# Kernel tuning notes

Hardware: AMD Instinct MI355X
Metric: run time of the kernel (lower is better)

## Reference

```python
import jax, jax.numpy as jnp
from jax import lax
import numpy as np

B, DIM, NH, H, W = 4, 256, 8, 32, 32
HEAD_DIM = DIM // NH          # 32
KEY_DIM = HEAD_DIM // 2       # attn_ratio = 0.5 -> 16
QKV_OUT = DIM + 2 * NH * KEY_DIM  # 512
SCALE = KEY_DIM ** -0.5


def setup_inputs() -> dict:
    key = jax.random.key(0)
    ks = jax.random.split(key, 11)
    w = lambda k, shape, s=0.05: jax.random.normal(k, shape, jnp.float32) * s
    return {
        "x": jax.random.normal(ks[0], (B, DIM, H, W), jnp.float32),
        "qkv_w": w(ks[1], (QKV_OUT, DIM)),
        "qkv_b": w(ks[2], (QKV_OUT,)),
        "proj_w": w(ks[3], (DIM, DIM)),
        "proj_b": w(ks[4], (DIM,)),
        "pe_w": w(ks[5], (DIM, 1, 3, 3)),
        "pe_b": w(ks[6], (DIM,)),
        "g1_w": w(ks[7], (DIM // 2, DIM)),
        "g1_b": w(ks[8], (DIM // 2,)),
        "g2_w": w(ks[9], (1, DIM // 2)),
        "g2_b": w(ks[10], (1,)),
    }


def conv1x1(x, w, b):
    # fused Conv2d(1x1, bias=False)+BN -> pointwise matmul + bias
    return jnp.einsum('bchw,oc->bohw', x, w) + b[None, :, None, None]


def reference(x, qkv_w, qkv_b, proj_w, proj_b, pe_w, pe_b, g1_w, g1_b, g2_w, g2_b):
    Bx, C, Hh, Ww = x.shape
    N = Hh * Ww
    qkv = conv1x1(x, qkv_w, qkv_b).reshape(Bx, NH, 2 * KEY_DIM + HEAD_DIM, N)
    q = qkv[:, :, :KEY_DIM]                   # [B, nh, key_dim, N]
    k = qkv[:, :, KEY_DIM:2 * KEY_DIM]        # [B, nh, key_dim, N]
    v = qkv[:, :, 2 * KEY_DIM:]               # [B, nh, head_dim, N]

    # attn = q^T @ k * scale  -> [B, nh, N, N]
    attn = jnp.einsum('bhdn,bhdm->bhnm', q, k) * SCALE

    # learned gate -> scalar dynamic k = floor(N * mean(sigmoid(...)))
    g = jax.nn.sigmoid(conv1x1(jax.nn.relu(conv1x1(x, g1_w, g1_b)), g2_w, g2_b))
    dyn_k = jnp.floor(N * jnp.mean(g)).astype(jnp.int32)

    # rank-based top-k mask (jit-friendly equivalent of topk+scatter):
    # keep entries whose descending rank along the last dim is < dyn_k
    order = jnp.argsort(-attn, axis=-1)       # positions sorted by score desc
    ranks = jnp.argsort(order, axis=-1)       # rank of each position
    attn = jnp.where(ranks < dyn_k, attn, -jnp.inf)
    attn = jax.nn.softmax(attn, axis=-1)

    out = jnp.einsum('bhdn,bhmn->bhdm', v, attn).reshape(Bx, C, Hh, Ww)

    # depthwise 3x3 positional-encoding conv on v reshaped to the image grid
    v_img = v.reshape(Bx, C, Hh, Ww)
    pe = lax.conv_general_dilated(
        v_img, pe_w, window_strides=(1, 1), padding=((1, 1), (1, 1)),
        dimension_numbers=('NCHW', 'OIHW', 'NCHW'), feature_group_count=C,
    ) + pe_b[None, :, None, None]

    return conv1x1(out + pe, proj_w, proj_b)
```

## Files before the change

### kernel.cpp

```cpp
#include <hip/hip_runtime.h>
#include <math.h>

#define NTOK 1024
#define CAP 64

#define LDS_FENCE() asm volatile("s_waitcnt lgkmcnt(0)" ::: "memory")

typedef __bf16 bf16x8 __attribute__((ext_vector_type(8)));
typedef unsigned short u16x8 __attribute__((ext_vector_type(8)));
typedef unsigned short u16x4 __attribute__((ext_vector_type(4)));
typedef float f32x4 __attribute__((ext_vector_type(4)));

__device__ __forceinline__ unsigned short f2bf(float f) {
  unsigned int u = __float_as_uint(f);
  return (unsigned short)((u + 0x7fffu + ((u >> 16) & 1u)) >> 16);
}


template<int OC, int OCB, int P, bool RELU, bool VCAST>
__global__ __launch_bounds__(256) void conv1x1_kernel(const float* __restrict__ in,
    const float* __restrict__ w, const float* __restrict__ bias, float* __restrict__ out,
    unsigned short* __restrict__ vbf) {
  constexpr int PB = NTOK / (256 * P);
  int bid = blockIdx.x;
  const int pb = bid % PB; bid /= PB;
  const int ocb = bid % (OC / OCB); const int b = bid / (OC / OCB);
  const int tid = threadIdx.x;
  const int p0 = pb * 256 * P + tid * P;
  const float* inb = in + (size_t)b * 256 * NTOK + p0;
  const float* wrow = w + (size_t)ocb * OCB * 256;

  float acc[OCB][P];
  #pragma unroll
  for (int j = 0; j < OCB; j++)
    #pragma unroll
    for (int i = 0; i < P; i++) acc[j][i] = 0.f;

  #pragma unroll 2
  for (int c0 = 0; c0 < 256; c0 += 4) {
    float4 wl[OCB];
    #pragma unroll
    for (int j = 0; j < OCB; j++) wl[j] = *(const float4*)&wrow[j * 256 + c0];
    #pragma unroll
    for (int cc = 0; cc < 4; cc++) {
      float xr[P];
      if constexpr (P == 4) {
        float4 t = *(const float4*)&inb[(size_t)(c0 + cc) * NTOK];
        xr[0] = t.x; xr[1] = t.y; xr[2] = t.z; xr[3] = t.w;
      } else if constexpr (P == 2) {
        float2 t = *(const float2*)&inb[(size_t)(c0 + cc) * NTOK];
        xr[0] = t.x; xr[1] = t.y;
      } else {
        xr[0] = inb[(size_t)(c0 + cc) * NTOK];
      }
      #pragma unroll
      for (int j = 0; j < OCB; j++) {
        const float wjc = ((const float*)&wl[j])[cc];
        #pragma unroll
        for (int i = 0; i < P; i++) acc[j][i] = fmaf(wjc, xr[i], acc[j][i]);
      }
    }
  }
  #pragma unroll
  for (int j = 0; j < OCB; j++) {
    const int oc = ocb * OCB + j;
    const float bv = bias[oc];
    float r[P];
    #pragma unroll
    for (int i = 0; i < P; i++) {
      float v = acc[j][i] + bv;
      if (RELU) v = fmaxf(v, 0.f);
      r[i] = v;
    }
    float* op = out + ((size_t)b * OC + oc) * NTOK + p0;
    if constexpr (P == 4) *(float4*)op = make_float4(r[0], r[1], r[2], r[3]);
    else if constexpr (P == 2) *(float2*)op = make_float2(r[0], r[1]);
    else *op = r[0];
    if constexpr (VCAST) {
      if ((oc & 63) >= 32) {
        const int c = (oc >> 6) * 32 + (oc & 63) - 32;
        unsigned short* vp = vbf + ((size_t)b * 256 + c) * NTOK + p0;
        #pragma unroll
        for (int i = 0; i < P; i++) vp[i] = f2bf(r[i]);
      }
    }
  }
}

__global__ __launch_bounds__(256) void gate2_kernel(const float* __restrict__ gx,
    const float* __restrict__ g2_w, const float* __restrict__ g2_b, double* __restrict__ part) {
  const int idx = blockIdx.x * 256 + threadIdx.x;
  const int b = idx >> 10, p = idx & 1023;
  float acc = g2_b[0];
  const float* gb = gx + (size_t)b * 128 * NTOK + p;
  #pragma unroll 4
  for (int j = 0; j < 128; j++) acc = fmaf(g2_w[j], gb[(size_t)j * NTOK], acc);
  float g = 1.f / (1.f + expf(-acc));
  __shared__ double red[256];
  red[threadIdx.x] = (double)g;
  __syncthreads();
  for (int s = 128; s > 0; s >>= 1) {
    if (threadIdx.x < s) red[threadIdx.x] += red[threadIdx.x + s];
    __syncthreads();
  }
  if (threadIdx.x == 0) part[blockIdx.x] = red[0];
}

__global__ __launch_bounds__(512) void attn_kernel(const float* __restrict__ qkv,
    const unsigned short* __restrict__ vbf,
    const double* __restrict__ part, float* __restrict__ out_attn) {
  const int tid = threadIdx.x;
  const int lane = tid & 63, wv = tid >> 6;
  int bid = blockIdx.x;
  const int mb = bid & 127; bid >>= 7;
  const int h = bid & 7; const int b = bid >> 3;

  double dsum = 0.0;
  #pragma unroll
  for (int i = 0; i < 16; i++) dsum += part[i];
  int dk = (int)floor(1024.0 * (dsum / 4096.0));
  const int dyn_k = dk < 1 ? 1 : (dk > NTOK ? NTOK : dk);

  const float* base = qkv + (size_t)(b * 512 + h * 64) * NTOK;

  __shared__ union RowU { float f[1028]; unsigned short pa[1032]; } rows[8];
  __shared__ float invs[8];
  __shared__ union UU {
    struct {
      int hist[8][64];
      int cnt[8];
      float Bv[8]; int Bn[8];
      struct { float v; int n; } cand[8][CAP];
    } sel;
    float pvred[2][4][8][17];
  } u;

  {
    const float2* k2 = (const float2*)(base + 16 * NTOK);
    const float* qb = base + mb * 8;
    float a0[8], a1[8];
    #pragma unroll
    for (int r = 0; r < 8; r++) { a0[r] = 0.f; a1[r] = 0.f; }
    #pragma unroll
    for (int d = 0; d < 16; d++) {
      float2 kk = k2[d * 512 + tid];
      #pragma unroll
      for (int r = 0; r < 8; r++) {
        const float qv = qb[(size_t)d * NTOK + r];
        a0[r] = fmaf(qv, kk.x, a0[r]);
        a1[r] = fmaf(qv, kk.y, a1[r]);
      }
    }
    #pragma unroll
    for (int r = 0; r < 8; r++)
      ((float2*)rows[r].f)[tid] = make_float2(a0[r] * 0.25f, a1[r] * 0.25f);
  }
  __syncthreads();

  {
    const int r = wv;
    float* smrow = rows[r].f;
    float v[16];
    {
      float4 f0 = ((const float4*)smrow)[lane];
      float4 f1 = ((const float4*)smrow)[64 + lane];
      float4 f2 = ((const float4*)smrow)[128 + lane];
      float4 f3 = ((const float4*)smrow)[192 + lane];
      v[0]=f0.x; v[1]=f0.y; v[2]=f0.z; v[3]=f0.w;
      v[4]=f1.x; v[5]=f1.y; v[6]=f1.z; v[7]=f1.w;
      v[8]=f2.x; v[9]=f2.y; v[10]=f2.z; v[11]=f2.w;
      v[12]=f3.x; v[13]=f3.y; v[14]=f3.z; v[15]=f3.w;
    }
    float mn = v[0], mx = v[0];
    #pragma unroll
    for (int i = 1; i < 16; i++) { mn = fminf(mn, v[i]); mx = fmaxf(mx, v[i]); }
    #pragma unroll
    for (int off = 32; off > 0; off >>= 1) {
      mn = fminf(mn, __shfl_xor(mn, off));
      mx = fmaxf(mx, __shfl_xor(mx, off));
    }

    unsigned int keepmask = 0xFFFFu;
    if (dyn_k < NTOK) {
      float Bv = mx; int Bn = dyn_k - 1;
      const float range = mx - mn;
      const bool fine = (range > 0.f);
      int m = 0;
      if (fine) {
        const float s1 = 64.0f / range;
        u.sel.hist[wv][lane] = 0;
        LDS_FENCE();
        int idx1[16];
        #pragma unroll
        for (int i = 0; i < 16; i++) {
          int ix = (int)((v[i] - mn) * s1);
          ix = ix < 0 ? 0 : (ix > 63 ? 63 : ix);
          idx1[i] = ix;
          atomicAdd(&u.sel.hist[wv][ix], 1);
        }
        LDS_FENCE();
        int cum = u.sel.hist[wv][lane];
        #pragma unroll
        for (int off = 1; off < 64; off <<= 1) {
          int o = __shfl_down(cum, off);
          if (lane + off < 64) cum += o;
        }
        int cumNext = __shfl_down(cum, 1);
        if (lane == 63) cumNext = 0;
        unsigned long long bal = __ballot(cum >= dyn_k && cumNext < dyn_k);
        const int t = (int)__builtin_ctzll(bal);
        const int k2 = dyn_k - __shfl(cumNext, t);
        const float binw = range * (1.0f / 64.0f);
        const float lo = mn + (float)t * binw;
        float s2 = 4096.0f / range;
        if (!(s2 < 3.0e38f)) s2 = 0.f;
        u.sel.hist[wv][lane] = 0;
        LDS_FENCE();
        #pragma unroll
        for (int i = 0; i < 16; i++) {
          if (idx1[i] == t) {
            int ix = (int)((v[i] - lo) * s2);
            ix = ix < 0 ? 0 : (ix > 63 ? 63 : ix);
            atomicAdd(&u.sel.hist[wv][ix], 1);
          }
        }
        LDS_FENCE();
        cum = u.sel.hist[wv][lane];
        #pragma unroll
        for (int off = 1; off < 64; off <<= 1) {
          int o = __shfl_down(cum, off);
          if (lane + off < 64) cum += o;
        }
        cumNext = __shfl_down(cum, 1);
        if (lane == 63) cumNext = 0;
        bal = __ballot(cum >= k2 && cumNext < k2);
        const int t2 = (int)__builtin_ctzll(bal);
        const int k3 = k2 - __shfl(cumNext, t2);
        if (lane == 0) u.sel.cnt[wv] = 0;
        LDS_FENCE();
        #pragma unroll
        for (int i = 0; i < 16; i++) {
          if (idx1[i] == t) {
            int ix = (int)((v[i] - lo) * s2);
            ix = ix < 0 ? 0 : (ix > 63 ? 63 : ix);
            if (ix == t2) {
              int p = atomicAdd(&u.sel.cnt[wv], 1);
              if (p < CAP) { u.sel.cand[wv][p].v = v[i]; u.sel.cand[wv][p].n = (i >> 2) * 256 + lane * 4 + (i & 3); }
            }
          }
        }
        LDS_FENCE();
        m = u.sel.cnt[wv];
        if (m <= CAP) {
          for (int ii = lane; ii < m; ii += 64) {
            float cv = u.sel.cand[wv][ii].v; int cn = u.sel.cand[wv][ii].n;
            int rk = 0;
            for (int j = 0; j < m; j++) {
              float ov = u.sel.cand[wv][j].v; int on = u.sel.cand[wv][j].n;
              rk += ((ov > cv) || (ov == cv && on < cn)) ? 1 : 0;
            }
            if (rk == k3 - 1) { u.sel.Bv[wv] = cv; u.sel.Bn[wv] = cn; }
          }
          LDS_FENCE();
          Bv = u.sel.Bv[wv]; Bn = u.sel.Bn[wv];
        }
      }
      if (fine && m > CAP) {
        keepmask = 0u;
        #pragma unroll
        for (int i = 0; i < 16; i++) {
          const int n_i = (i >> 2) * 256 + lane * 4 + (i & 3);
          const float vi = v[i];
          int rk = 0;
          for (int j = 0; j < NTOK; j++) {
            float ov = smrow[j];
            rk += ((ov > vi) || (ov == vi && j < n_i)) ? 1 : 0;
          }
          if (rk < dyn_k) keepmask |= (1u << i);
        }
      } else {
        keepmask = 0u;
        #pragma unroll
        for (int i = 0; i < 16; i++) {
          const int n_i = (i >> 2) * 256 + lane * 4 + (i & 3);
          if ((v[i] > Bv) || (v[i] == Bv && n_i <= Bn)) keepmask |= (1u << i);
        }
      }
    }
    float e[16]; float s = 0.f;
    #pragma unroll
    for (int i = 0; i < 16; i++) {
      e[i] = ((keepmask >> i) & 1u) ? __expf(v[i] - mx) : 0.f;
      s += e[i];
    }
    #pragma unroll
    for (int off = 32; off > 0; off >>= 1) s += __shfl_xor(s, off);
    if (lane == 0) invs[r] = 1.f / s;
    #pragma unroll
    for (int j = 0; j < 4; j++) {
      u16x4 w4 = { f2bf(e[4*j]), f2bf(e[4*j+1]), f2bf(e[4*j+2]), f2bf(e[4*j+3]) };
      *(u16x4*)&rows[r].pa[j * 256 + lane * 4] = w4;
    }
  }
  __syncthreads();

  {
    const int g = lane >> 4;
    const int m16 = lane & 15;
    const int ksl = wv & 3, dt = wv >> 2;
    const unsigned short* vrow = vbf + ((size_t)(b * 256 + h * 32 + dt * 16 + m16)) * NTOK;
    const unsigned short* parow = rows[lane & 7].pa;
    f32x4 acc = {0.f, 0.f, 0.f, 0.f};
    const int nb = ksl * 256;
    #pragma unroll
    for (int ks = 0; ks < 8; ks++) {
      const int n0 = nb + ks * 32 + g * 8;
      bf16x8 a  = __builtin_bit_cast(bf16x8, *(const u16x8*)&parow[n0]);
      bf16x8 b0 = __builtin_bit_cast(bf16x8, *(const u16x8*)&vrow[n0]);
      acc = __builtin_amdgcn_mfma_f32_16x16x32_bf16(a, b0, acc, 0, 0, 0);
    }
    if (g < 2) {
      #pragma unroll
      for (int q = 0; q < 4; q++)
        u.pvred[dt][ksl][g * 4 + q][m16] = acc[q];
    }
  }
  __syncthreads();
  if (tid < 256) {
    const int r2 = tid & 7, d2 = tid >> 3;
    const int dt = d2 >> 4, m16 = d2 & 15;
    float s = u.pvred[dt][0][r2][m16] + u.pvred[dt][1][r2][m16]
            + u.pvred[dt][2][r2][m16] + u.pvred[dt][3][r2][m16];
    s *= invs[r2];
    out_attn[(size_t)(b * 256 + h * 32 + d2) * NTOK + mb * 8 + r2] = s;
  }
}

__global__ __launch_bounds__(256) void pe_kernel(const float* __restrict__ qkv,
    const float* __restrict__ oattn, const float* __restrict__ pe_w,
    const float* __restrict__ pe_b, float* __restrict__ tmp) {
  int bid = blockIdx.x;
  const int c = bid & 255; const int b = bid >> 8;
  const int oc = ((c >> 5) * 64) + 32 + (c & 31);
  const float* vimg = qkv + (size_t)(b * 512 + oc) * NTOK;
  float wloc[9];
  #pragma unroll
  for (int i = 0; i < 9; i++) wloc[i] = pe_w[c * 9 + i];
  const float bv = pe_b[c];
  const float* oa = oattn + (size_t)(b * 256 + c) * NTOK;
  float* tp = tmp + (size_t)(b * 256 + c) * NTOK;
  for (int p = threadIdx.x; p < NTOK; p += 256) {
    const int y = p >> 5, x = p & 31;
    float s = bv;
    #pragma unroll
    for (int dy = -1; dy <= 1; dy++) {
      int yy = y + dy;
      if (yy < 0 || yy > 31) continue;
      #pragma unroll
      for (int dx = -1; dx <= 1; dx++) {
        int xx = x + dx;
        if (xx < 0 || xx > 31) continue;
        s = fmaf(wloc[(dy + 1) * 3 + (dx + 1)], vimg[yy * 32 + xx], s);
      }
    }
    tp[p] = s + oa[p];
  }
}

extern "C" void kernel_launch(void* const* d_in, const int* in_sizes, int n_in,
                              void* d_out, int out_size, void* d_ws, size_t ws_size,
                              hipStream_t stream) {
  const float* x      = (const float*)d_in[0];
  const float* qkv_w  = (const float*)d_in[1];
  const float* qkv_b  = (const float*)d_in[2];
  const float* proj_w = (const float*)d_in[3];
  const float* proj_b = (const float*)d_in[4];
  const float* pe_w   = (const float*)d_in[5];
  const float* pe_b   = (const float*)d_in[6];
  const float* g1_w   = (const float*)d_in[7];
  const float* g1_b   = (const float*)d_in[8];
  const float* g2_w   = (const float*)d_in[9];
  const float* g2_b   = (const float*)d_in[10];
  float* out = (float*)d_out;

  char* ws = (char*)d_ws;
  float*  qkvb  = (float*)(ws);
  float*  oattn = (float*)(ws + (8u << 20));
  float*  tmp   = (float*)(ws + (12u << 20));
  float*  gx    = (float*)(ws + (16u << 20));
  unsigned short* vbf = (unsigned short*)(ws + (16u << 20));
  double* part  = (double*)(ws + (18u << 20));

  conv1x1_kernel<128, 2, 2, true, false><<<512, 256, 0, stream>>>(x, g1_w, g1_b, gx, nullptr);
  gate2_kernel<<<16, 256, 0, stream>>>(gx, g2_w, g2_b, part);
  conv1x1_kernel<512, 8, 2, false, true><<<512, 256, 0, stream>>>(x, qkv_w, qkv_b, qkvb, vbf);
  attn_kernel<<<4096, 512, 0, stream>>>(qkvb, vbf, part, oattn);
  pe_kernel<<<1024, 256, 0, stream>>>(qkvb, oattn, pe_w, pe_b, tmp);
  conv1x1_kernel<256, 4, 2, false, false><<<512, 256, 0, stream>>>(tmp, proj_w, proj_b, out, nullptr);
}
```

Measured before the change: 165.8 us.

## Fuse gate conv layers into one kernel and precompute dynamic k once

Fuses the gate's first 1x1 conv with ReLU and the second 1x1 conv plus sigmoid into a single kernel. The 128-channel hidden activations stay in shared memory and never round-trip through global memory. Adds a one-block kernel that reduces the gate values and writes dyn_k, so each of the 4096 attention blocks reads one int instead of summing 16 doubles. It also changes the launch structure: the gate stage now uses 256 blocks and adds a serial single-block reduction launch.

```diff
diff --git a/kernel.cpp b/kernel.cpp
--- a/kernel.cpp
+++ b/kernel.cpp
@@ -87,39 +87,71 @@
   }
 }
 
-__global__ __launch_bounds__(256) void gate2_kernel(const float* __restrict__ gx,
-    const float* __restrict__ g2_w, const float* __restrict__ g2_b, double* __restrict__ part) {
-  const int idx = blockIdx.x * 256 + threadIdx.x;
-  const int b = idx >> 10, p = idx & 1023;
-  float acc = g2_b[0];
-  const float* gb = gx + (size_t)b * 128 * NTOK + p;
-  #pragma unroll 4
-  for (int j = 0; j < 128; j++) acc = fmaf(g2_w[j], gb[(size_t)j * NTOK], acc);
-  float g = 1.f / (1.f + expf(-acc));
+__global__ __launch_bounds__(256) void gate12_kernel(const float* __restrict__ x,
+    const float* __restrict__ g1_w, const float* __restrict__ g1_b,
+    const float* __restrict__ g2_w, const float* __restrict__ g2_b,
+    float* __restrict__ gvals) {
+  const int tid = threadIdx.x;
+  const int p_l = tid & 15, jg = tid >> 4;
+  const int pb = blockIdx.x & 63, b = blockIdx.x >> 6;
+  const float* xb = x + (size_t)b * 256 * NTOK + pb * 16 + p_l;
+  const float* w1 = g1_w + (size_t)jg * 8 * 256;
+  __shared__ float hs[128][17];
+
+  float acc[8];
+  #pragma unroll
+  for (int jj = 0; jj < 8; jj++) acc[jj] = g1_b[jg * 8 + jj];
+  #pragma unroll 2
+  for (int c0 = 0; c0 < 256; c0 += 4) {
+    float xr[4];
+    #pragma unroll
+    for (int cc = 0; cc < 4; cc++) xr[cc] = xb[(size_t)(c0 + cc) * NTOK];
+    #pragma unroll
+    for (int jj = 0; jj < 8; jj++) {
+      const float4 w4 = *(const float4*)&w1[jj * 256 + c0];
+      acc[jj] = fmaf(w4.x, xr[0], acc[jj]);
+      acc[jj] = fmaf(w4.y, xr[1], acc[jj]);
+      acc[jj] = fmaf(w4.z, xr[2], acc[jj]);
+      acc[jj] = fmaf(w4.w, xr[3], acc[jj]);
+    }
+  }
+  #pragma unroll
+  for (int jj = 0; jj < 8; jj++) hs[jg * 8 + jj][p_l] = fmaxf(acc[jj], 0.f);
+  __syncthreads();
+  if (tid < 16) {
+    float a = g2_b[0];
+    for (int j = 0; j < 128; j++) a = fmaf(g2_w[j], hs[j][tid], a);
+    gvals[(size_t)b * NTOK + pb * 16 + tid] = 1.f / (1.f + expf(-a));
+  }
+}
+
+__global__ void dynk_kernel(const float* __restrict__ gvals, int* __restrict__ dynk) {
+  const int t = threadIdx.x;
+  double s = 0.0;
+  #pragma unroll
+  for (int i = 0; i < 16; i++) s += (double)gvals[t + 256 * i];
   __shared__ double red[256];
-  red[threadIdx.x] = (double)g;
+  red[t] = s;
   __syncthreads();
-  for (int s = 128; s > 0; s >>= 1) {
-    if (threadIdx.x < s) red[threadIdx.x] += red[threadIdx.x + s];
+  for (int st = 128; st > 0; st >>= 1) {
+    if (t < st) red[t] += red[t + st];
     __syncthreads();
   }
-  if (threadIdx.x == 0) part[blockIdx.x] = red[0];
+  if (t == 0) {
+    int k = (int)floor(1024.0 * (red[0] / 4096.0));
+    *dynk = k < 1 ? 1 : (k > NTOK ? NTOK : k);
+  }
 }
 
 __global__ __launch_bounds__(512) void attn_kernel(const float* __restrict__ qkv,
     const unsigned short* __restrict__ vbf,
-    const double* __restrict__ part, float* __restrict__ out_attn) {
+    const int* __restrict__ dynk_p, float* __restrict__ out_attn) {
   const int tid = threadIdx.x;
   const int lane = tid & 63, wv = tid >> 6;
   int bid = blockIdx.x;
   const int mb = bid & 127; bid >>= 7;
   const int h = bid & 7; const int b = bid >> 3;
-
-  double dsum = 0.0;
-  #pragma unroll
-  for (int i = 0; i < 16; i++) dsum += part[i];
-  int dk = (int)floor(1024.0 * (dsum / 4096.0));
-  const int dyn_k = dk < 1 ? 1 : (dk > NTOK ? NTOK : dk);
+  const int dyn_k = *dynk_p;
 
   const float* base = qkv + (size_t)(b * 512 + h * 64) * NTOK;
 
@@ -387,14 +419,14 @@
   float*  qkvb  = (float*)(ws);
   float*  oattn = (float*)(ws + (8u << 20));
   float*  tmp   = (float*)(ws + (12u << 20));
-  float*  gx    = (float*)(ws + (16u << 20));
   unsigned short* vbf = (unsigned short*)(ws + (16u << 20));
-  double* part  = (double*)(ws + (18u << 20));
-
-  conv1x1_kernel<128, 2, 2, true, false><<<512, 256, 0, stream>>>(x, g1_w, g1_b, gx, nullptr);
-  gate2_kernel<<<16, 256, 0, stream>>>(gx, g2_w, g2_b, part);
+  float*  gvals = (float*)(ws + (18u << 20));
+  int*    dynk  = (int*)(ws + (18u << 20) + (64u << 10));
+
+  gate12_kernel<<<256, 256, 0, stream>>>(x, g1_w, g1_b, g2_w, g2_b, gvals);
+  dynk_kernel<<<1, 256, 0, stream>>>(gvals, dynk);
   conv1x1_kernel<512, 8, 2, false, true><<<512, 256, 0, stream>>>(x, qkv_w, qkv_b, qkvb, vbf);
-  attn_kernel<<<4096, 512, 0, stream>>>(qkvb, vbf, part, oattn);
+  attn_kernel<<<4096, 512, 0, stream>>>(qkvb, vbf, dynk, oattn);
   pe_kernel<<<1024, 256, 0, stream>>>(qkvb, oattn, pe_w, pe_b, tmp);
   conv1x1_kernel<256, 4, 2, false, false><<<512, 256, 0, stream>>>(tmp, proj_w, proj_b, out, nullptr);
 }
```

Result: slower. 171.5 us (+3.4%).
